# Kernel tuning notes

Hardware: AMD Instinct MI355X
Metric: run time of the kernel (lower is better)

## Reference

```python
import jax, jax.numpy as jnp
import numpy as np


def setup_inputs() -> dict:
    key = jax.random.key(0)
    k1, k2 = jax.random.split(key)
    p1 = jax.random.normal(k1, (4, 8192, 3), dtype=jnp.float32)
    p2 = jax.random.normal(k2, (4, 8192, 3), dtype=jnp.float32)
    return {"p1": p1, "p2": p2}


def reference(p1, p2):
    # dist[b, n, m] = ||p1[b, n] - p2[b, m]||^2  (faithful to broadcasted diff)
    diff = p1[:, :, None, :] - p2[:, None, :, :]          # [B, N, M, 3]
    dist = jnp.sum(diff * diff, axis=-1)                  # [B, N, M]
    p1_to_p2 = jnp.min(dist, axis=-1)                     # [B, N]
    p2_to_p1 = jnp.min(dist, axis=-2)                     # [B, M]
    chamfer = (p1_to_p2.mean(axis=-1) + p2_to_p1.mean(axis=-1)).mean()
    return chamfer
```

## Files before the change

kernel.cpp:

```cpp
#include <hip/hip_runtime.h>

#define THREADS 256
#define QPT 16
#define Q2  (QPT / 2)
#define SLICES 64
#define NPTS 8192
#define BATCH 4
#define SLICE (NPTS / SLICES)

typedef float f2 __attribute__((ext_vector_type(2)));
typedef float f4 __attribute__((ext_vector_type(4)));


__global__ void chamfer_init(unsigned int* mins, float* out) {
    int i = blockIdx.x * blockDim.x + threadIdx.x;
    mins[i] = 0x7F800000u;
    if (i == 0) out[0] = 0.0f;
}

__global__ __launch_bounds__(THREADS, 4) void chamfer_main(
    const float* __restrict__ p1, const float* __restrict__ p2,
    unsigned int* __restrict__ mins)
{
    const int tid  = threadIdx.x;
    const int bz   = blockIdx.z;
    const int dir  = bz >> 2;
    const int b    = bz & 3;
    const int qbase = blockIdx.x * (THREADS * QPT);
    const int tbase = blockIdx.y * SLICE;

    const float* __restrict__ qsrc = (dir == 0) ? p1 : p2;
    const float* __restrict__ tsrc = (dir == 0) ? p2 : p1;

    __shared__ f4 tgt[SLICE];
    {
        const float* tp = tsrc + ((size_t)b * NPTS + tbase) * 3;
        for (int k = tid; k < SLICE; k += THREADS) {
            float x = tp[k * 3 + 0];
            float y = tp[k * 3 + 1];
            float z = tp[k * 3 + 2];
            tgt[k] = f4{-2.0f * x, -2.0f * y, -2.0f * z,
                        fmaf(x, x, fmaf(y, y, z * z))};
        }
    }

    f2 ax2[Q2], ay2[Q2], az2[Q2], a2q[Q2], best2[Q2];
#pragma unroll
    for (int j = 0; j < Q2; ++j) {
        const int qa = qbase + (2 * j + 0) * THREADS + tid;
        const int qb = qbase + (2 * j + 1) * THREADS + tid;
        const float* pa = qsrc + ((size_t)b * NPTS + qa) * 3;
        const float* pb = qsrc + ((size_t)b * NPTS + qb) * 3;
        ax2[j] = f2{pa[0], pb[0]};
        ay2[j] = f2{pa[1], pb[1]};
        az2[j] = f2{pa[2], pb[2]};
        a2q[j].x = fmaf(ax2[j].x, ax2[j].x, fmaf(ay2[j].x, ay2[j].x, az2[j].x * az2[j].x));
        a2q[j].y = fmaf(ax2[j].y, ax2[j].y, fmaf(ay2[j].y, ay2[j].y, az2[j].y * az2[j].y));
        best2[j] = f2{3.0e38f, 3.0e38f};
    }

    __syncthreads();

#pragma unroll 4
    for (int m = 0; m < SLICE; m += 2) {
        f4 ta = tgt[m];
        f4 tb = tgt[m + 1];
        f2 ta_xy = __builtin_shufflevector(ta, ta, 0, 1);
        f2 ta_zw = __builtin_shufflevector(ta, ta, 2, 3);
        f2 tb_xy = __builtin_shufflevector(tb, tb, 0, 1);
        f2 tb_zw = __builtin_shufflevector(tb, tb, 2, 3);
#pragma unroll
        for (int j = 0; j < Q2; ++j) {
            f2 da, db;
            asm("v_pk_fma_f32 %0, %1, %2, %2 op_sel:[0,0,1] op_sel_hi:[1,0,1]"
                : "=v"(da) : "v"(az2[j]), "v"(ta_zw));
            asm("v_pk_fma_f32 %0, %1, %2, %0 op_sel:[0,1,0] op_sel_hi:[1,1,1]"
                : "+v"(da) : "v"(ay2[j]), "v"(ta_xy));
            asm("v_pk_fma_f32 %0, %1, %2, %0 op_sel:[0,0,0] op_sel_hi:[1,0,1]"
                : "+v"(da) : "v"(ax2[j]), "v"(ta_xy));
            asm("v_pk_fma_f32 %0, %1, %2, %2 op_sel:[0,0,1] op_sel_hi:[1,0,1]"
                : "=v"(db) : "v"(az2[j]), "v"(tb_zw));
            asm("v_pk_fma_f32 %0, %1, %2, %0 op_sel:[0,1,0] op_sel_hi:[1,1,1]"
                : "+v"(db) : "v"(ay2[j]), "v"(tb_xy));
            asm("v_pk_fma_f32 %0, %1, %2, %0 op_sel:[0,0,0] op_sel_hi:[1,0,1]"
                : "+v"(db) : "v"(ax2[j]), "v"(tb_xy));
            best2[j].x = fminf(fminf(best2[j].x, da.x), db.x);
            best2[j].y = fminf(fminf(best2[j].y, da.y), db.y);
        }
    }

    unsigned int* mbase = mins + ((size_t)dir * BATCH + b) * NPTS;
#pragma unroll
    for (int j = 0; j < Q2; ++j) {
        float va = fmaxf(best2[j].x + a2q[j].x, 0.0f);
        float vb = fmaxf(best2[j].y + a2q[j].y, 0.0f);
        atomicMin(&mbase[qbase + (2 * j + 0) * THREADS + tid], __float_as_uint(va));
        atomicMin(&mbase[qbase + (2 * j + 1) * THREADS + tid], __float_as_uint(vb));
    }
}

__global__ __launch_bounds__(THREADS) void chamfer_reduce(
    const uint4* __restrict__ mins, float* __restrict__ out)
{
    const int i = blockIdx.x * THREADS + threadIdx.x;
    uint4 u = mins[i];
    float s = __uint_as_float(u.x) + __uint_as_float(u.y)
            + __uint_as_float(u.z) + __uint_as_float(u.w);
#pragma unroll
    for (int off = 32; off >= 1; off >>= 1)
        s += __shfl_down(s, off, 64);
    __shared__ float partial[THREADS / 64];
    if ((threadIdx.x & 63) == 0) partial[threadIdx.x >> 6] = s;
    __syncthreads();
    if (threadIdx.x == 0) {
        float tot = 0.0f;
#pragma unroll
        for (int w = 0; w < THREADS / 64; ++w) tot += partial[w];
        atomicAdd(out, tot * (1.0f / (BATCH * NPTS)));
    }
}

extern "C" void kernel_launch(void* const* d_in, const int* in_sizes, int n_in,
                              void* d_out, int out_size, void* d_ws, size_t ws_size,
                              hipStream_t stream) {
    const float* p1 = (const float*)d_in[0];
    const float* p2 = (const float*)d_in[1];
    unsigned int* mins = (unsigned int*)d_ws;
    float* out = (float*)d_out;

    chamfer_init<<<(2 * BATCH * NPTS) / THREADS, THREADS, 0, stream>>>(mins, out);

    dim3 grid(NPTS / (THREADS * QPT), SLICES, 2 * BATCH);
    chamfer_main<<<grid, THREADS, 0, stream>>>(p1, p2, mins);

    chamfer_reduce<<<(2 * BATCH * NPTS) / (4 * THREADS), THREADS, 0, stream>>>(
        (const uint4*)mins, out);
}
```

Baseline: 101.6 us.

## Fuse final reduction into main kernel via last-block counter; halve queries per thread

Adds a global atomic ticket counter so the last finishing block of the main kernel sums all per-point minima and writes the output, removing the separate reduce launch when the workspace has room for the counter. Queries per thread drop from 16 to 8, which doubles the grid and lowers register use, and the query-norm computation moves to the epilogue to free more registers. The cost is one extra fence and atomic per block, plus a serial single-block reduction over 65K values at the tail of the kernel.

```diff
diff --git a/kernel.cpp b/kernel.cpp
--- a/kernel.cpp
+++ b/kernel.cpp
@@ -1,26 +1,29 @@
 #include <hip/hip_runtime.h>
 
 #define THREADS 256
-#define QPT 16
+#define QPT 8
 #define Q2  (QPT / 2)
 #define SLICES 64
 #define NPTS 8192
 #define BATCH 4
 #define SLICE (NPTS / SLICES)
+#define NMINS (2 * BATCH * NPTS)
+#define NBLOCKS ((NPTS / (THREADS * QPT)) * SLICES * 2 * BATCH)
 
 typedef float f2 __attribute__((ext_vector_type(2)));
 typedef float f4 __attribute__((ext_vector_type(4)));
 
 
-__global__ void chamfer_init(unsigned int* mins, float* out) {
+__global__ void chamfer_init(unsigned int* mins, unsigned int* counter) {
     int i = blockIdx.x * blockDim.x + threadIdx.x;
     mins[i] = 0x7F800000u;
-    if (i == 0) out[0] = 0.0f;
+    if (i == 0 && counter) *counter = 0u;
 }
 
 __global__ __launch_bounds__(THREADS, 4) void chamfer_main(
     const float* __restrict__ p1, const float* __restrict__ p2,
-    unsigned int* __restrict__ mins)
+    unsigned int* __restrict__ mins, unsigned int* __restrict__ counter,
+    float* __restrict__ out)
 {
     const int tid  = threadIdx.x;
     const int bz   = blockIdx.z;
@@ -44,7 +47,7 @@
         }
     }
 
-    f2 ax2[Q2], ay2[Q2], az2[Q2], a2q[Q2], best2[Q2];
+    f2 ax2[Q2], ay2[Q2], az2[Q2], best2[Q2];
 #pragma unroll
     for (int j = 0; j < Q2; ++j) {
         const int qa = qbase + (2 * j + 0) * THREADS + tid;
@@ -54,14 +57,12 @@
         ax2[j] = f2{pa[0], pb[0]};
         ay2[j] = f2{pa[1], pb[1]};
         az2[j] = f2{pa[2], pb[2]};
-        a2q[j].x = fmaf(ax2[j].x, ax2[j].x, fmaf(ay2[j].x, ay2[j].x, az2[j].x * az2[j].x));
-        a2q[j].y = fmaf(ax2[j].y, ax2[j].y, fmaf(ay2[j].y, ay2[j].y, az2[j].y * az2[j].y));
         best2[j] = f2{3.0e38f, 3.0e38f};
     }
 
     __syncthreads();
 
-#pragma unroll 4
+#pragma unroll 2
     for (int m = 0; m < SLICE; m += 2) {
         f4 ta = tgt[m];
         f4 tb = tgt[m + 1];
@@ -92,10 +93,40 @@
     unsigned int* mbase = mins + ((size_t)dir * BATCH + b) * NPTS;
 #pragma unroll
     for (int j = 0; j < Q2; ++j) {
-        float va = fmaxf(best2[j].x + a2q[j].x, 0.0f);
-        float vb = fmaxf(best2[j].y + a2q[j].y, 0.0f);
+        float qa2 = fmaf(ax2[j].x, ax2[j].x, fmaf(ay2[j].x, ay2[j].x, az2[j].x * az2[j].x));
+        float qb2 = fmaf(ax2[j].y, ax2[j].y, fmaf(ay2[j].y, ay2[j].y, az2[j].y * az2[j].y));
+        float va = fmaxf(best2[j].x + qa2, 0.0f);
+        float vb = fmaxf(best2[j].y + qb2, 0.0f);
         atomicMin(&mbase[qbase + (2 * j + 0) * THREADS + tid], __float_as_uint(va));
         atomicMin(&mbase[qbase + (2 * j + 1) * THREADS + tid], __float_as_uint(vb));
+    }
+
+    if (counter) {
+        __threadfence();
+        __syncthreads();
+        __shared__ unsigned int tick;
+        if (tid == 0)
+            tick = __hip_atomic_fetch_add(counter, 1u, __ATOMIC_ACQ_REL,
+                                          __HIP_MEMORY_SCOPE_AGENT);
+        __syncthreads();
+        if (tick == NBLOCKS - 1) {
+            float s = 0.0f;
+            for (int i = tid; i < NMINS; i += THREADS) {
+                unsigned int u = __hip_atomic_load(&mins[i], __ATOMIC_RELAXED,
+                                                   __HIP_MEMORY_SCOPE_AGENT);
+                s += __uint_as_float(u);
+            }
+#pragma unroll
+            for (int off = 32; off >= 1; off >>= 1)
+                s += __shfl_down(s, off, 64);
+            __shared__ float part[THREADS / 64];
+            if ((tid & 63) == 0) part[tid >> 6] = s;
+            __syncthreads();
+            if (tid == 0) {
+                float tot = part[0] + part[1] + part[2] + part[3];
+                out[0] = tot * (1.0f / (BATCH * NPTS));
+            }
+        }
     }
 }
 
@@ -127,12 +158,15 @@
     const float* p2 = (const float*)d_in[1];
     unsigned int* mins = (unsigned int*)d_ws;
     float* out = (float*)d_out;
+    const bool fused = ws_size >= (size_t)(NMINS + 1) * sizeof(unsigned int);
+    unsigned int* counter = fused ? (mins + NMINS) : nullptr;
 
-    chamfer_init<<<(2 * BATCH * NPTS) / THREADS, THREADS, 0, stream>>>(mins, out);
+    chamfer_init<<<NMINS / THREADS, THREADS, 0, stream>>>(mins, counter);
 
     dim3 grid(NPTS / (THREADS * QPT), SLICES, 2 * BATCH);
-    chamfer_main<<<grid, THREADS, 0, stream>>>(p1, p2, mins);
+    chamfer_main<<<grid, THREADS, 0, stream>>>(p1, p2, mins, counter, out);
 
-    chamfer_reduce<<<(2 * BATCH * NPTS) / (4 * THREADS), THREADS, 0, stream>>>(
-        (const uint4*)mins, out);
+    if (!fused)
+        chamfer_reduce<<<NMINS / (4 * THREADS), THREADS, 0, stream>>>(
+            (const uint4*)mins, out);
 }
```

Result: slower. 274.5 us (+170.3%).
